# Kernel tuning notes

Measured on AMD Instinct MI355X. Metric: run time of the kernel, lower is better.

Reference implementation:

```python
import jax, jax.numpy as jnp
import numpy as np

B, LTMS, TTS, C_IN, F, H = 64, 16, 256, 128, 256, 256


def setup_inputs() -> dict:
    key = jax.random.key(0)
    ks = jax.random.split(key, 6)
    s = 0.05  # small init keeps relu-GRU numerically tame
    return {
        "x": jax.random.normal(ks[0], (B, LTMS * TTS, C_IN), dtype=jnp.float32),
        "conv_w": jax.random.normal(ks[1], (1, C_IN, F), dtype=jnp.float32) * s,
        "conv_b": jnp.zeros((F,), dtype=jnp.float32),
        "attn_w": jax.random.normal(ks[2], (TTS, TTS), dtype=jnp.float32) * s,
        "attn_b": jnp.zeros((TTS,), dtype=jnp.float32),
        "gru_w": jax.random.normal(ks[3], (F, 3 * H), dtype=jnp.float32) * s,
        "gru_u": jax.random.normal(ks[4], (H, 3 * H), dtype=jnp.float32) * s,
        "gru_b": jnp.zeros((2, 3 * H), dtype=jnp.float32),
    }


def _forward(x, conv_w, conv_b, attn_w, attn_b, gru_w, gru_u, gru_b):
    b = x.shape[0]
    # [B, LTMS*TTS, C] -> [B*LTMS, TTS, C]; segments are independent, so the
    # original per-segment Python loop vectorizes into the leading batch dim.
    xs = x.reshape(b * LTMS, TTS, C_IN)
    # Conv1D kernel_size=1 == pointwise GEMM, then ReLU (dropout=0 at inference)
    conv = jax.nn.relu(jnp.einsum('ntc,cf->ntf', xs, conv_w[0]) + conv_b)  # [N,T,F]
    # Attention: softmax(Dense) over time axis per filter, multiply back
    xt = conv.transpose(0, 2, 1)                                  # [N,F,T]
    probs = jax.nn.softmax(xt @ attn_w + attn_b, axis=-1)         # [N,F,T]
    x_att = conv * probs.transpose(0, 2, 1)                       # [N,T,F]
    # GRU (keras v2, reset_after=True), activation=relu, gate order z,r,h
    bi, br = gru_b[0], gru_b[1]
    gates_x = x_att @ gru_w + bi                                  # [N,T,3H]
    def step(h, gx):
        rec = h @ gru_u + br
        xz, xr, xh = jnp.split(gx, 3, axis=-1)
        rz, rr, rh = jnp.split(rec, 3, axis=-1)
        z = jax.nn.sigmoid(xz + rz)
        r = jax.nn.sigmoid(xr + rr)
        hh = jax.nn.relu(xh + r * rh)
        h_new = z * h + (1.0 - z) * hh
        return h_new, None
    h0 = jnp.zeros((b * LTMS, H), dtype=x.dtype)
    h_final, _ = jax.lax.scan(step, h0, gates_x.transpose(1, 0, 2))
    return h_final.reshape(b, LTMS, H)


def reference(x, conv_w, conv_b, attn_w, attn_b, gru_w, gru_u, gru_b):
    return _forward(x, conv_w, conv_b, attn_w, attn_b, gru_w, gru_u, gru_b)
```

## Files before the change

kernel.cpp:

```cpp
#include <hip/hip_runtime.h>
#include <stdint.h>

typedef unsigned short u16;
typedef __attribute__((ext_vector_type(8))) __bf16 bf16x8;
typedef __attribute__((ext_vector_type(4))) float f32x4;

#define TTS 256
#define NSEG 1024
#define TC 32

__device__ __forceinline__ u16 f2bf(float f) {
  union { float f; uint32_t u; } v; v.f = f;
  uint32_t r = v.u + 0x7fffu + ((v.u >> 16) & 1u);
  return (u16)(r >> 16);
}
__device__ __forceinline__ float bf2f(u16 h) {
  union { uint32_t u; float f; } v; v.u = ((uint32_t)h) << 16;
  return v.f;
}
__device__ __forceinline__ float sigm(float x) {
  return __builtin_amdgcn_rcpf(1.0f + __expf(-x));
}
__device__ __forceinline__ void gl16(const void* g, void* l) {
  __builtin_amdgcn_global_load_lds(
      (const __attribute__((address_space(1))) unsigned int*)g,
      (__attribute__((address_space(3))) unsigned int*)l, 16, 0, 0);
}

__global__ void k_transp(const float* __restrict__ in, u16* __restrict__ out, int R, int C) {
  int i = blockIdx.x * blockDim.x + threadIdx.x;
  if (i < R * C) {
    int r = i / C, c = i % C;
    out[(size_t)c * R + r] = f2bf(in[i]);
  }
}

template <bool RELU, bool STORE_T, int AMODE>
__global__ __launch_bounds__(512, 4) void k_gemm(
    const void* __restrict__ Av, const u16* __restrict__ Bt,
    const float* __restrict__ bias, u16* __restrict__ out, int K, int Nld, int t0) {
  __shared__ __attribute__((aligned(16))) u16 ldsA[4096];
  __shared__ __attribute__((aligned(16))) u16 ldsB[8192];
  const int tid  = threadIdx.x;
  const int w    = tid >> 6;
  const int lane = tid & 63;
  const int quad = lane >> 4;
  const int l16  = lane & 15;
  const int m0 = blockIdx.x * 128;
  const int n0 = blockIdx.y * 256;
  const int wm = w >> 2, wn = w & 3;
  const int arow = tid & 127, ac = tid >> 7;

  f32x4 acc[4][4];
#pragma unroll
  for (int i = 0; i < 4; i++)
#pragma unroll
    for (int j = 0; j < 4; j++) acc[i][j] = f32x4{0.f, 0.f, 0.f, 0.f};

  for (int k0 = 0; k0 < K; k0 += 32) {
    ushort4 va0, va1;
    if (AMODE == 0) {
      const float* Af = (const float*)Av;
      const float* p = Af + (size_t)(m0 + arow) * K + k0 + ac * 8;
      float4 f0 = *(const float4*)p;
      float4 f1 = *(const float4*)(p + 4);
      va0 = ushort4{f2bf(f0.x), f2bf(f0.y), f2bf(f0.z), f2bf(f0.w)};
      va1 = ushort4{f2bf(f1.x), f2bf(f1.y), f2bf(f1.z), f2bf(f1.w)};
    }
    __syncthreads();
    if (AMODE == 0) {
      *(ushort4*)&ldsA[tid * 8]     = va0;
      *(ushort4*)&ldsA[tid * 8 + 4] = va1;
    } else {
      const u16* Ax = (const u16*)Av;
      int r = m0 + arow;
      int kk = k0 + ac * 8;
      gl16(Ax + (size_t)(r >> 5) * 65536 + (size_t)(kk >> 6) * 16384 +
               (t0 + (r & 31)) * 64 + (kk & 63),
           &ldsA[tid * 8]);
    }
#pragma unroll
    for (int i = 0; i < 2; i++) {
      int idx = i * 512 + tid;
      int brow = idx & 255, bc = idx >> 8;
      gl16(Bt + (size_t)(n0 + brow) * K + k0 + bc * 8, &ldsB[idx * 8]);
    }
    __syncthreads();
    bf16x8 a[4], b[4];
#pragma unroll
    for (int i = 0; i < 4; i++)
      a[i] = *(const bf16x8*)&ldsA[(quad * 128 + wm * 64 + i * 16 + l16) * 8];
#pragma unroll
    for (int j = 0; j < 4; j++)
      b[j] = *(const bf16x8*)&ldsB[(quad * 256 + wn * 64 + j * 16 + l16) * 8];
#pragma unroll
    for (int i = 0; i < 4; i++)
#pragma unroll
      for (int j = 0; j < 4; j++)
        acc[i][j] = __builtin_amdgcn_mfma_f32_16x16x32_bf16(a[i], b[j], acc[i][j], 0, 0, 0);
  }

#pragma unroll
  for (int j = 0; j < 4; j++) {
    int col = n0 + wn * 64 + j * 16 + l16;
    float bv = bias[col];
#pragma unroll
    for (int i = 0; i < 4; i++) {
      int row0 = m0 + wm * 64 + i * 16 + quad * 4;
      if (STORE_T) {
        int nseg = row0 >> 8, tt0 = row0 & 255;
        ushort4 o;
        float v0 = acc[i][j][0] + bv, v1 = acc[i][j][1] + bv;
        float v2 = acc[i][j][2] + bv, v3 = acc[i][j][3] + bv;
        if (RELU) {
          v0 = fmaxf(v0, 0.f); v1 = fmaxf(v1, 0.f);
          v2 = fmaxf(v2, 0.f); v3 = fmaxf(v3, 0.f);
        }
        o.x = f2bf(v0); o.y = f2bf(v1); o.z = f2bf(v2); o.w = f2bf(v3);
        *(ushort4*)&out[(size_t)nseg * 65536 + (size_t)(col >> 6) * 16384 +
                        (col & 63) * 256 + tt0] = o;
      } else {
#pragma unroll
        for (int r = 0; r < 4; r++) {
          float v = acc[i][j][r] + bv;
          if (RELU) v = fmaxf(v, 0.f);
          out[(size_t)(row0 + r) * Nld + col] = f2bf(v);
        }
      }
    }
  }
}

__global__ __launch_bounds__(256) void k_attn(
    u16* xac,
    const u16* __restrict__ Wt,
    const float* __restrict__ attn_b) {
  __shared__ u16 ldsW[8192];
  __shared__ u16 ldsC[16384];
  __shared__ float redmax[4][64];
  __shared__ float redsum[4][64];
  const int tid  = threadIdx.x;
  const int w    = tid >> 6;
  const int lane = tid & 63;
  const int quad = lane >> 4;
  const int l16  = lane & 15;
  const int seg = blockIdx.x;
  const int c4  = blockIdx.y;
  u16* reg = xac + (size_t)seg * 65536 + (size_t)c4 * 16384;

  {
    const int f = tid & 63, g = tid >> 6;
#pragma unroll
    for (int u = 0; u < 8; u++) {
      int tch = g * 8 + u;
      *(bf16x8*)&ldsC[(tch * 64 + f) * 8] =
          *(const bf16x8*)(reg + (size_t)f * 256 + tch * 8);
    }
  }

  f32x4 acc[4][4];
#pragma unroll
  for (int i = 0; i < 4; i++)
#pragma unroll
    for (int j = 0; j < 4; j++) acc[i][j] = f32x4{0.f, 0.f, 0.f, 0.f};

  for (int s = 0; s < 8; s++) {
    int k0 = s * 32;
    bf16x8 vw[4];
#pragma unroll
    for (int c = 0; c < 4; c++)
      vw[c] = *(const bf16x8*)(Wt + (size_t)tid * 256 + k0 + c * 8);
    __syncthreads();
#pragma unroll
    for (int c = 0; c < 4; c++)
      *(bf16x8*)&ldsW[(c * 256 + tid) * 8] = vw[c];
    __syncthreads();
    bf16x8 a[4], b[4];
#pragma unroll
    for (int i = 0; i < 4; i++)
      a[i] = *(const bf16x8*)&ldsW[(quad * 256 + w * 64 + i * 16 + l16) * 8];
#pragma unroll
    for (int j = 0; j < 4; j++)
      b[j] = *(const bf16x8*)&ldsC[((s * 4 + quad) * 64 + j * 16 + l16) * 8];
#pragma unroll
    for (int i = 0; i < 4; i++)
#pragma unroll
      for (int j = 0; j < 4; j++)
        acc[i][j] = __builtin_amdgcn_mfma_f32_16x16x32_bf16(a[i], b[j], acc[i][j], 0, 0, 0);
  }

#pragma unroll
  for (int i = 0; i < 4; i++)
#pragma unroll
    for (int r = 0; r < 4; r++) {
      float ab = attn_b[w * 64 + i * 16 + quad * 4 + r];
#pragma unroll
      for (int j = 0; j < 4; j++) acc[i][j][r] += ab;
    }

  float lmax[4];
#pragma unroll
  for (int j = 0; j < 4; j++) {
    float m = -1e30f;
#pragma unroll
    for (int i = 0; i < 4; i++)
#pragma unroll
      for (int r = 0; r < 4; r++) m = fmaxf(m, acc[i][j][r]);
    m = fmaxf(m, __shfl_xor(m, 16));
    m = fmaxf(m, __shfl_xor(m, 32));
    lmax[j] = m;
  }
  __syncthreads();
  if (quad == 0) {
#pragma unroll
    for (int j = 0; j < 4; j++) redmax[w][j * 16 + l16] = lmax[j];
  }
  __syncthreads();
  float gmax[4];
#pragma unroll
  for (int j = 0; j < 4; j++) {
    int c = j * 16 + l16;
    gmax[j] = fmaxf(fmaxf(redmax[0][c], redmax[1][c]), fmaxf(redmax[2][c], redmax[3][c]));
  }
  float lsum[4];
#pragma unroll
  for (int j = 0; j < 4; j++) {
    float sacc = 0.f;
#pragma unroll
    for (int i = 0; i < 4; i++)
#pragma unroll
      for (int r = 0; r < 4; r++) {
        float e = __expf(acc[i][j][r] - gmax[j]);
        acc[i][j][r] = e;
        sacc += e;
      }
    sacc += __shfl_xor(sacc, 16);
    sacc += __shfl_xor(sacc, 32);
    lsum[j] = sacc;
  }
  if (quad == 0) {
#pragma unroll
    for (int j = 0; j < 4; j++) redsum[w][j * 16 + l16] = lsum[j];
  }
  __syncthreads();
  float rinv[4];
#pragma unroll
  for (int j = 0; j < 4; j++) {
    int c = j * 16 + l16;
    rinv[j] = 1.0f / (redsum[0][c] + redsum[1][c] + redsum[2][c] + redsum[3][c]);
  }

#pragma unroll
  for (int i = 0; i < 4; i++) {
#pragma unroll
    for (int r = 0; r < 4; r++) {
      int tp = w * 64 + i * 16 + quad * 4 + r;
#pragma unroll
      for (int j = 0; j < 4; j++) {
        int fl = j * 16 + l16;
        float cv = bf2f(ldsC[((tp >> 3) * 64 + fl) * 8 + (tp & 7)]);
        float xa = acc[i][j][r] * rinv[j] * cv;
        reg[(size_t)tp * 64 + fl] = f2bf(xa);
      }
    }
  }
}

__global__ __launch_bounds__(512, 2) void k_scanc(
    const u16* __restrict__ gc,
    const u16* __restrict__ Ut,
    const float* __restrict__ br,
    float* __restrict__ hio,
    int init) {
  __shared__ u16 uls[65536];
  __shared__ u16 hb[16 * 264];
  const int tid  = threadIdx.x;
  const int w    = tid >> 6;
  const int lane = tid & 63;
  const int quad = lane >> 4;
  const int l16  = lane & 15;
  const int n0 = blockIdx.x * 16;
  const int cg[2] = {w, 8 + w};

#pragma unroll
  for (int j = 0; j < 2; j++)
#pragma unroll
    for (int s = 0; s < 8; s++)
      *(bf16x8*)&uls[w * 8192 + (j * 8 + s) * 512 + lane * 8] =
          *(const bf16x8*)(Ut + (size_t)(j * 256 + cg[1] * 16 + l16) * 256 + s * 32 + quad * 8);

  bf16x8 ur0[3][8], urh1[8];
#pragma unroll
  for (int g = 0; g < 3; g++)
#pragma unroll
    for (int s = 0; s < 8; s++)
      ur0[g][s] = *(const bf16x8*)(Ut + (size_t)(g * 256 + cg[0] * 16 + l16) * 256 + s * 32 + quad * 8);
#pragma unroll
  for (int s = 0; s < 8; s++)
    urh1[s] = *(const bf16x8*)(Ut + (size_t)(512 + cg[1] * 16 + l16) * 256 + s * 32 + quad * 8);

  float brZ[2], brR[2], brH[2];
#pragma unroll
  for (int grp = 0; grp < 2; grp++) {
    int c = cg[grp] * 16 + l16;
    brZ[grp] = br[c]; brR[grp] = br[256 + c]; brH[grp] = br[512 + c];
  }

  float hreg[2][4];
#pragma unroll
  for (int grp = 0; grp < 2; grp++)
#pragma unroll
    for (int r = 0; r < 4; r++)
      hreg[grp][r] = init ? 0.f
                          : hio[(size_t)(n0 + quad * 4 + r) * 256 + cg[grp] * 16 + l16];
  {
    int sg = tid >> 5, c0 = (tid & 31) * 8;
    if (init) {
      *(ushort4*)&hb[sg * 264 + c0]     = ushort4{0, 0, 0, 0};
      *(ushort4*)&hb[sg * 264 + c0 + 4] = ushort4{0, 0, 0, 0};
    } else {
      const float* hp = hio + (size_t)(n0 + sg) * 256 + c0;
      float4 h0 = *(const float4*)(hp), h1 = *(const float4*)(hp + 4);
      *(ushort4*)&hb[sg * 264 + c0]     = ushort4{f2bf(h0.x), f2bf(h0.y), f2bf(h0.z), f2bf(h0.w)};
      *(ushort4*)&hb[sg * 264 + c0 + 4] = ushort4{f2bf(h1.x), f2bf(h1.y), f2bf(h1.z), f2bf(h1.w)};
    }
  }
  const u16* gseg[4];
#pragma unroll
  for (int r = 0; r < 4; r++)
    gseg[r] = gc + (size_t)(n0 + quad * 4 + r) * TC * 768;
  __syncthreads();

  for (int tt = 0; tt < TC; tt++) {
    float gg[2][3][4];
#pragma unroll
    for (int grp = 0; grp < 2; grp++)
#pragma unroll
      for (int g = 0; g < 3; g++)
#pragma unroll
        for (int r = 0; r < 4; r++)
          gg[grp][g][r] = bf2f(gseg[r][tt * 768 + g * 256 + cg[grp] * 16 + l16]);

    f32x4 acc[2][3];
#pragma unroll
    for (int grp = 0; grp < 2; grp++)
#pragma unroll
      for (int g = 0; g < 3; g++) acc[grp][g] = f32x4{0.f, 0.f, 0.f, 0.f};

#pragma unroll
    for (int s = 0; s < 8; s++) {
      bf16x8 ah = *(const bf16x8*)&hb[l16 * 264 + s * 32 + quad * 8];
#pragma unroll
      for (int g = 0; g < 3; g++)
        acc[0][g] = __builtin_amdgcn_mfma_f32_16x16x32_bf16(ah, ur0[g][s], acc[0][g], 0, 0, 0);
      bf16x8 uz = *(const bf16x8*)&uls[w * 8192 + s * 512 + lane * 8];
      bf16x8 urr = *(const bf16x8*)&uls[w * 8192 + (8 + s) * 512 + lane * 8];
      acc[1][0] = __builtin_amdgcn_mfma_f32_16x16x32_bf16(ah, uz,      acc[1][0], 0, 0, 0);
      acc[1][1] = __builtin_amdgcn_mfma_f32_16x16x32_bf16(ah, urr,     acc[1][1], 0, 0, 0);
      acc[1][2] = __builtin_amdgcn_mfma_f32_16x16x32_bf16(ah, urh1[s], acc[1][2], 0, 0, 0);
    }
    __syncthreads();

#pragma unroll
    for (int grp = 0; grp < 2; grp++)
#pragma unroll
      for (int r = 0; r < 4; r++) {
        float z  = sigm(acc[grp][0][r] + gg[grp][0][r] + brZ[grp]);
        float rg = sigm(acc[grp][1][r] + gg[grp][1][r] + brR[grp]);
        float hh = fmaxf(gg[grp][2][r] + rg * (acc[grp][2][r] + brH[grp]), 0.f);
        float hn = z * hreg[grp][r] + (1.0f - z) * hh;
        hreg[grp][r] = hn;
        hb[(quad * 4 + r) * 264 + cg[grp] * 16 + l16] = f2bf(hn);
      }
    __syncthreads();
  }

#pragma unroll
  for (int grp = 0; grp < 2; grp++)
#pragma unroll
    for (int r = 0; r < 4; r++)
      hio[(size_t)(n0 + quad * 4 + r) * 256 + cg[grp] * 16 + l16] = hreg[grp][r];
}

extern "C" void kernel_launch(void* const* d_in, const int* in_sizes, int n_in,
                              void* d_out, int out_size, void* d_ws, size_t ws_size,
                              hipStream_t stream) {
  (void)in_sizes; (void)n_in; (void)out_size;
  const float* x      = (const float*)d_in[0];
  const float* conv_w = (const float*)d_in[1];
  const float* conv_b = (const float*)d_in[2];
  const float* attn_w = (const float*)d_in[3];
  const float* attn_b = (const float*)d_in[4];
  const float* gru_w  = (const float*)d_in[5];
  const float* gru_u  = (const float*)d_in[6];
  const float* gru_b  = (const float*)d_in[7];

  const size_t NEEDED = 185532416;
  if (ws_size < NEEDED) return;
  char* ws = (char*)d_ws;
  u16* xac     = (u16*)(ws);
  u16* gatesC  = (u16*)(ws + 134217728);
  u16* conv_wT = (u16*)(ws + 184549376);
  u16* attn_wT = (u16*)(ws + 184614912);
  u16* gru_wT  = (u16*)(ws + 184745984);
  u16* gru_uT  = (u16*)(ws + 185139200);

  hipLaunchKernelGGL(k_transp, dim3(128), dim3(256), 0, stream, conv_w, conv_wT, 128, 256);
  hipLaunchKernelGGL(k_transp, dim3(256), dim3(256), 0, stream, attn_w, attn_wT, 256, 256);
  hipLaunchKernelGGL(k_transp, dim3(768), dim3(256), 0, stream, gru_w, gru_wT, 256, 768);
  hipLaunchKernelGGL(k_transp, dim3(768), dim3(256), 0, stream, gru_u, gru_uT, 256, 768);

  hipLaunchKernelGGL((k_gemm<true, true, 0>), dim3(2048, 1), dim3(512), 0, stream,
                     (const void*)x, conv_wT, conv_b, xac, 128, 0, 0);
  hipLaunchKernelGGL(k_attn, dim3(1024, 4), dim3(256), 0, stream,
                     xac, attn_wT, attn_b);
  for (int c = 0; c < 8; c++) {
    hipLaunchKernelGGL((k_gemm<false, false, 1>), dim3(256, 3), dim3(512), 0, stream,
                       (const void*)xac, gru_wT, gru_b, gatesC, 256, 768, c * TC);
    hipLaunchKernelGGL(k_scanc, dim3(64), dim3(512), 0, stream,
                       gatesC, gru_uT, gru_b + 768, (float*)d_out, c == 0 ? 1 : 0);
  }
}
```

Before: 1.243 ms.

## Double-buffer GEMM LDS tiles and load attention weights directly from global

The GEMM kernel now uses two LDS buffers, prefetching the next K-slice (global-to-LDS for B and bf16 A, register prefetch for fp32 A) while MFMAs run on the current slice. This needs only one barrier per iteration, at the cost of doubled LDS use and an occupancy hint lowered from 4 to 2. The attention kernel drops its LDS staging of the weight matrix, reads A fragments straight from global/L2, and fully unrolls the loop, which removes two barriers per step. That trades LDS traffic and syncs for uncoalesced global reads of a small shared weight.

```diff
diff --git a/kernel.cpp b/kernel.cpp
--- a/kernel.cpp
+++ b/kernel.cpp
@@ -36,11 +36,11 @@
 }
 
 template <bool RELU, bool STORE_T, int AMODE>
-__global__ __launch_bounds__(512, 4) void k_gemm(
+__global__ __launch_bounds__(512, 2) void k_gemm(
     const void* __restrict__ Av, const u16* __restrict__ Bt,
     const float* __restrict__ bias, u16* __restrict__ out, int K, int Nld, int t0) {
-  __shared__ __attribute__((aligned(16))) u16 ldsA[4096];
-  __shared__ __attribute__((aligned(16))) u16 ldsB[8192];
+  __shared__ __attribute__((aligned(16))) u16 ldsA[2][4096];
+  __shared__ __attribute__((aligned(16))) u16 ldsB[2][8192];
   const int tid  = threadIdx.x;
   const int w    = tid >> 6;
   const int lane = tid & 63;
@@ -50,6 +50,8 @@
   const int n0 = blockIdx.y * 256;
   const int wm = w >> 2, wn = w & 3;
   const int arow = tid & 127, ac = tid >> 7;
+  const float* Af = (const float*)Av;
+  const u16*   Ax = (const u16*)Av;
 
   f32x4 acc[4][4];
 #pragma unroll
@@ -57,47 +59,68 @@
 #pragma unroll
     for (int j = 0; j < 4; j++) acc[i][j] = f32x4{0.f, 0.f, 0.f, 0.f};
 
+  float4 p0, p1;
+  if (AMODE == 0) {
+    const float* p = Af + (size_t)(m0 + arow) * K + ac * 8;
+    p0 = *(const float4*)p;
+    p1 = *(const float4*)(p + 4);
+  } else {
+    int r = m0 + arow, kk = ac * 8;
+    gl16(Ax + (size_t)(r >> 5) * 65536 + (size_t)(kk >> 6) * 16384 +
+             (t0 + (r & 31)) * 64 + (kk & 63),
+         &ldsA[0][tid * 8]);
+  }
+#pragma unroll
+  for (int i = 0; i < 2; i++) {
+    int idx = i * 512 + tid, brow = idx & 255, bc = idx >> 8;
+    gl16(Bt + (size_t)(n0 + brow) * K + bc * 8, &ldsB[0][idx * 8]);
+  }
+  if (AMODE == 0) {
+    *(ushort4*)&ldsA[0][tid * 8]     = ushort4{f2bf(p0.x), f2bf(p0.y), f2bf(p0.z), f2bf(p0.w)};
+    *(ushort4*)&ldsA[0][tid * 8 + 4] = ushort4{f2bf(p1.x), f2bf(p1.y), f2bf(p1.z), f2bf(p1.w)};
+  }
+  __syncthreads();
+
+  int cur = 0;
   for (int k0 = 0; k0 < K; k0 += 32) {
-    ushort4 va0, va1;
-    if (AMODE == 0) {
-      const float* Af = (const float*)Av;
-      const float* p = Af + (size_t)(m0 + arow) * K + k0 + ac * 8;
-      float4 f0 = *(const float4*)p;
-      float4 f1 = *(const float4*)(p + 4);
-      va0 = ushort4{f2bf(f0.x), f2bf(f0.y), f2bf(f0.z), f2bf(f0.w)};
-      va1 = ushort4{f2bf(f1.x), f2bf(f1.y), f2bf(f1.z), f2bf(f1.w)};
-    }
-    __syncthreads();
-    if (AMODE == 0) {
-      *(ushort4*)&ldsA[tid * 8]     = va0;
-      *(ushort4*)&ldsA[tid * 8 + 4] = va1;
-    } else {
-      const u16* Ax = (const u16*)Av;
-      int r = m0 + arow;
-      int kk = k0 + ac * 8;
-      gl16(Ax + (size_t)(r >> 5) * 65536 + (size_t)(kk >> 6) * 16384 +
-               (t0 + (r & 31)) * 64 + (kk & 63),
-           &ldsA[tid * 8]);
-    }
-#pragma unroll
-    for (int i = 0; i < 2; i++) {
-      int idx = i * 512 + tid;
-      int brow = idx & 255, bc = idx >> 8;
-      gl16(Bt + (size_t)(n0 + brow) * K + k0 + bc * 8, &ldsB[idx * 8]);
-    }
-    __syncthreads();
+    const int kn = k0 + 32;
+    const bool more = kn < K;
+    float4 q0, q1;
+    if (more) {
+      if (AMODE == 0) {
+        const float* p = Af + (size_t)(m0 + arow) * K + kn + ac * 8;
+        q0 = *(const float4*)p;
+        q1 = *(const float4*)(p + 4);
+      } else {
+        int r = m0 + arow, kk = kn + ac * 8;
+        gl16(Ax + (size_t)(r >> 5) * 65536 + (size_t)(kk >> 6) * 16384 +
+                 (t0 + (r & 31)) * 64 + (kk & 63),
+             &ldsA[cur ^ 1][tid * 8]);
+      }
+#pragma unroll
+      for (int i = 0; i < 2; i++) {
+        int idx = i * 512 + tid, brow = idx & 255, bc = idx >> 8;
+        gl16(Bt + (size_t)(n0 + brow) * K + kn + bc * 8, &ldsB[cur ^ 1][idx * 8]);
+      }
+    }
     bf16x8 a[4], b[4];
 #pragma unroll
     for (int i = 0; i < 4; i++)
-      a[i] = *(const bf16x8*)&ldsA[(quad * 128 + wm * 64 + i * 16 + l16) * 8];
+      a[i] = *(const bf16x8*)&ldsA[cur][(quad * 128 + wm * 64 + i * 16 + l16) * 8];
 #pragma unroll
     for (int j = 0; j < 4; j++)
-      b[j] = *(const bf16x8*)&ldsB[(quad * 256 + wn * 64 + j * 16 + l16) * 8];
+      b[j] = *(const bf16x8*)&ldsB[cur][(quad * 256 + wn * 64 + j * 16 + l16) * 8];
 #pragma unroll
     for (int i = 0; i < 4; i++)
 #pragma unroll
       for (int j = 0; j < 4; j++)
         acc[i][j] = __builtin_amdgcn_mfma_f32_16x16x32_bf16(a[i], b[j], acc[i][j], 0, 0, 0);
+    if (AMODE == 0 && more) {
+      *(ushort4*)&ldsA[cur ^ 1][tid * 8]     = ushort4{f2bf(q0.x), f2bf(q0.y), f2bf(q0.z), f2bf(q0.w)};
+      *(ushort4*)&ldsA[cur ^ 1][tid * 8 + 4] = ushort4{f2bf(q1.x), f2bf(q1.y), f2bf(q1.z), f2bf(q1.w)};
+    }
+    __syncthreads();
+    cur ^= 1;
   }
 
 #pragma unroll
@@ -131,11 +154,10 @@
   }
 }
 
-__global__ __launch_bounds__(256) void k_attn(
+__global__ __launch_bounds__(256, 4) void k_attn(
     u16* xac,
     const u16* __restrict__ Wt,
     const float* __restrict__ attn_b) {
-  __shared__ u16 ldsW[8192];
   __shared__ u16 ldsC[16384];
   __shared__ float redmax[4][64];
   __shared__ float redsum[4][64];
@@ -157,6 +179,7 @@
           *(const bf16x8*)(reg + (size_t)f * 256 + tch * 8);
     }
   }
+  __syncthreads();
 
   f32x4 acc[4][4];
 #pragma unroll
@@ -164,21 +187,13 @@
 #pragma unroll
     for (int j = 0; j < 4; j++) acc[i][j] = f32x4{0.f, 0.f, 0.f, 0.f};
 
+#pragma unroll
   for (int s = 0; s < 8; s++) {
     int k0 = s * 32;
-    bf16x8 vw[4];
-#pragma unroll
-    for (int c = 0; c < 4; c++)
-      vw[c] = *(const bf16x8*)(Wt + (size_t)tid * 256 + k0 + c * 8);
-    __syncthreads();
-#pragma unroll
-    for (int c = 0; c < 4; c++)
-      *(bf16x8*)&ldsW[(c * 256 + tid) * 8] = vw[c];
-    __syncthreads();
     bf16x8 a[4], b[4];
 #pragma unroll
     for (int i = 0; i < 4; i++)
-      a[i] = *(const bf16x8*)&ldsW[(quad * 256 + w * 64 + i * 16 + l16) * 8];
+      a[i] = *(const bf16x8*)(Wt + (size_t)(w * 64 + i * 16 + l16) * 256 + k0 + quad * 8);
 #pragma unroll
     for (int j = 0; j < 4; j++)
       b[j] = *(const bf16x8*)&ldsC[((s * 4 + quad) * 64 + j * 16 + l16) * 8];
@@ -210,7 +225,6 @@
     m = fmaxf(m, __shfl_xor(m, 32));
     lmax[j] = m;
   }
-  __syncthreads();
   if (quad == 0) {
 #pragma unroll
     for (int j = 0; j < 4; j++) redmax[w][j * 16 + l16] = lmax[j];
```

After: 1.239 ms. About the same (-0.3%).
